# Optimization experiments

Measured on AMD Instinct MI355X. Metric: run time of the kernel, lower is better.

Reference implementation:

```python
import jax, jax.numpy as jnp
import numpy as np

L = 12; D = 768; H = 12; HD = D // H
P = 16; IMG = 224; NPATCH = (IMG // P) ** 2
NCLS = 1000; B = 32
GAMMA = 0.01; MIN_TOKENS = 16; EPS = 1e-6
SCALE = HD ** -0.5


def _ln(x, w, b, eps=1e-6):
    mu = x.mean(-1, keepdims=True)
    var = ((x - mu) ** 2).mean(-1, keepdims=True)
    return (x - mu) * jax.lax.rsqrt(var + eps) * w + b


def setup_inputs() -> dict:
    key = jax.random.key(0)
    ks = jax.random.split(key, 16)
    s = 0.02
    rn = lambda k, shape: jax.random.normal(k, shape, jnp.float32) * s
    return {
        'x': jax.random.normal(ks[0], (B, 3, IMG, IMG), jnp.float32),
        'patch_w': rn(ks[1], (D, 3, P, P)),
        'patch_b': jnp.zeros((D,), jnp.float32),
        'cls_token': rn(ks[2], (1, 1, D)),
        'pos_embed': rn(ks[3], (1, NPATCH + 1, D)),
        'ln1_w': jnp.ones((L, D), jnp.float32), 'ln1_b': jnp.zeros((L, D), jnp.float32),
        'qkv_w': rn(ks[4], (L, D, 3 * D)), 'qkv_b': jnp.zeros((L, 3 * D), jnp.float32),
        'proj_w': rn(ks[5], (L, D, D)), 'proj_b': jnp.zeros((L, D), jnp.float32),
        'ln2_w': jnp.ones((L, D), jnp.float32), 'ln2_b': jnp.zeros((L, D), jnp.float32),
        'fc1_w': rn(ks[6], (L, D, 4 * D)), 'fc1_b': jnp.zeros((L, 4 * D), jnp.float32),
        'fc2_w': rn(ks[7], (L, 4 * D, D)), 'fc2_b': jnp.zeros((L, D), jnp.float32),
        'norm_w': jnp.ones((D,), jnp.float32), 'norm_b': jnp.zeros((D,), jnp.float32),
        'head_w': rn(ks[8], (D, NCLS)), 'head_b': jnp.zeros((NCLS,), jnp.float32),
    }


def _block(x, i, ln1_w, ln1_b, qkv_w, qkv_b, proj_w, proj_b, ln2_w, ln2_b, fc1_w, fc1_b, fc2_w, fc2_b):
    Bb, Ntok, _ = x.shape
    xn = _ln(x, ln1_w[i], ln1_b[i])
    qkv = (xn @ qkv_w[i] + qkv_b[i]).reshape(Bb, Ntok, 3, H, HD)
    qkv = qkv.transpose(2, 0, 3, 1, 4)  # [3, B, H, N, hd]
    q, k, v = qkv[0], qkv[1], qkv[2]
    # full N x N attention matrix, materialized as in the original module
    attn = jax.nn.softmax(jnp.einsum('bhqd,bhkd->bhqk', q, k) * SCALE, axis=-1)
    out = jnp.einsum('bhqk,bhkd->bhqd', attn, v)
    out = out.transpose(0, 2, 1, 3).reshape(Bb, Ntok, D) @ proj_w[i] + proj_b[i]
    x = x + out
    h = _ln(x, ln2_w[i], ln2_b[i])
    h = jax.nn.gelu(h @ fc1_w[i] + fc1_b[i], approximate=False)
    x = x + (h @ fc2_w[i] + fc2_b[i])
    return x, attn, v


def _importance(attn, v, eps):
    # Jacobian proxy: d(CLS)/d(patch_j) ~ attn[CLS->j] * ||v_j||
    v_norm = jnp.linalg.norm(v, axis=-1)            # [B, H, N]
    jac = attn[:, :, 0, 1:] * v_norm[:, :, 1:]       # [B, H, Npatch]
    importance = jac.mean(axis=(0, 1))               # batch-shared [Npatch]
    mass = importance.sum()
    rho = importance.std() / (importance.mean() + eps)
    return importance, mass, rho


def _keep_ratio(rho, mass, prev_mass, gamma, eps):
    drift = jnp.abs(mass - prev_mass) / (prev_mass + eps)
    return jnp.clip(1.0 - gamma * rho * (1.0 + drift), 0.0, 1.0)


def _select(importance, n_keep):
    _, idx = jax.lax.top_k(importance, n_keep)
    idx = jnp.sort(idx) + 1  # shift past CLS
    return jnp.concatenate([jnp.zeros((1,), idx.dtype), idx])  # always keep CLS


def reference(x, patch_w, patch_b, cls_token, pos_embed, ln1_w, ln1_b, qkv_w, qkv_b,
              proj_w, proj_b, ln2_w, ln2_b, fc1_w, fc1_b, fc2_w, fc2_b,
              norm_w, norm_b, head_w, head_b):
    Bb = x.shape[0]
    feat = jax.lax.conv_general_dilated(x, patch_w, (P, P), 'VALID',
                                        dimension_numbers=('NCHW', 'OIHW', 'NCHW'))
    feat = feat.reshape(Bb, D, NPATCH).transpose(0, 2, 1) + patch_b  # [B, 196, D]
    xx = jnp.concatenate([jnp.broadcast_to(cls_token, (Bb, 1, D)), feat], axis=1) + pos_embed
    N = NPATCH
    prev_mass = None
    for i in range(L):
        xx, attn, v = _block(xx, i, ln1_w, ln1_b, qkv_w, qkv_b, proj_w, proj_b,
                             ln2_w, ln2_b, fc1_w, fc1_b, fc2_w, fc2_b)
        if N <= MIN_TOKENS:
            prev_mass = None
            continue
        imp, mass, rho = _importance(attn, v, EPS)
        if prev_mass is not None:
            kr = float(_keep_ratio(rho, mass, prev_mass, GAMMA, EPS))
            n_next = max(MIN_TOKENS, int(N * kr))
        else:
            n_next = N
        if n_next < N:
            keep_idx = _select(imp, n_next)
            xx = jnp.take(xx, keep_idx, axis=1)
            N = n_next
        prev_mass = mass
    xx = _ln(xx, norm_w, norm_b)
    return xx[:, 0] @ head_w + head_b
```

## Files before the change

kernel.cpp:

```cpp
#include <hip/hip_runtime.h>
#include <math.h>

#define DEV_INLINE __device__ __forceinline__

constexpr int BB     = 32;
constexpr int DMODEL = 768;
constexpr int NHEAD  = 12;
constexpr int NPATCH = 196;
constexpr int NTOK   = 197;
constexpr int NLAYER = 12;
constexpr int NCLASS = 1000;
constexpr int MTOT   = BB * NTOK;

typedef __attribute__((ext_vector_type(4))) float f32x4;
typedef __attribute__((ext_vector_type(8))) short bf16x8;

DEV_INLINE void split2(float x, unsigned short& hi, unsigned short& lo) {
    unsigned u = __builtin_bit_cast(unsigned, x);
    unsigned r = (u + 0x7FFFu + ((u >> 16) & 1u)) >> 16;
    hi = (unsigned short)r;
    float fh = __builtin_bit_cast(float, r << 16);
    float l = x - fh;
    unsigned ul = __builtin_bit_cast(unsigned, l);
    lo = (unsigned short)((ul + 0x7FFFu + ((ul >> 16) & 1u)) >> 16);
}

DEV_INLINE unsigned split_pack(float x) {
    unsigned short h, l; split2(x, h, l);
    return (unsigned)h | ((unsigned)l << 16);
}

DEV_INLINE void gload16(const unsigned short* g, unsigned short* l) {
    __builtin_amdgcn_global_load_lds(
        (const __attribute__((address_space(1))) unsigned int*)g,
        (__attribute__((address_space(3))) unsigned int*)l, 16, 0, 0);
}

DEV_INLINE float block_reduce_sum(float v, float* sbuf) {
    #pragma unroll
    for (int off = 32; off > 0; off >>= 1) v += __shfl_down(v, off, 64);
    int lane = threadIdx.x & 63, w = threadIdx.x >> 6;
    __syncthreads();
    if (lane == 0) sbuf[w] = v;
    __syncthreads();
    return sbuf[0] + sbuf[1] + sbuf[2] + sbuf[3];
}

__global__ void state_init(int* nTokPtr, int* prevValidPtr) {
    *nTokPtr = NTOK;
    *prevValidPtr = 0;
}

__global__ __launch_bounds__(256)
void cls_init(const float* __restrict__ cls, const float* __restrict__ pos,
              float* __restrict__ tok) {
    int b = blockIdx.x;
    for (int i = threadIdx.x; i < DMODEL; i += 256)
        tok[(size_t)b * NTOK * DMODEL + i] = cls[i] + pos[i];
}

__global__ __launch_bounds__(256)
void wconv_patch(const float* __restrict__ src, unsigned short* __restrict__ hi,
                 unsigned short* __restrict__ lo) {
    int id = blockIdx.x * 256 + threadIdx.x;
    if (id >= 768 * 96) return;
    int n = id / 96, ch = id % 96;
    int k = ch * 8;
    float4 a = *(const float4*)(src + (size_t)n * 768 + k);
    float4 b = *(const float4*)(src + (size_t)n * 768 + k + 4);
    unsigned short h[8], l[8];
    split2(a.x,h[0],l[0]); split2(a.y,h[1],l[1]); split2(a.z,h[2],l[2]); split2(a.w,h[3],l[3]);
    split2(b.x,h[4],l[4]); split2(b.y,h[5],l[5]); split2(b.z,h[6],l[6]); split2(b.w,h[7],l[7]);
    int npanel = n >> 7, c = n & 127;
    int kbi = k >> 5, chunk = (k >> 3) & 3;
    size_t base = ((size_t)npanel * 24 + kbi) * 4096
                + c * 32 + ((chunk ^ ((c >> 1) & 3)) << 3);
    bf16x8 hv, lv;
    #pragma unroll
    for (int j = 0; j < 8; ++j) { hv[j] = (short)h[j]; lv[j] = (short)l[j]; }
    *(bf16x8*)(hi + base) = hv;
    *(bf16x8*)(lo + base) = lv;
}

constexpr size_t WOFF_QKV  = 0;
constexpr size_t WOFF_PROJ = (size_t)768 * 2304;
constexpr size_t WOFF_FC1  = WOFF_PROJ + (size_t)768 * 768;
constexpr size_t WOFF_FC2  = WOFF_FC1 + (size_t)768 * 3072;
constexpr size_t WTOTAL    = WOFF_FC2 + (size_t)3072 * 768;

__global__ __launch_bounds__(256)
void wconv_layer(const float* __restrict__ qkvw, const float* __restrict__ projw,
                 const float* __restrict__ fc1w, const float* __restrict__ fc2w,
                 unsigned short* __restrict__ hi, unsigned short* __restrict__ lo) {
    __shared__ float tile[32][33];
    int bid = blockIdx.x;
    const float* src; int Kd, Nd; size_t dofs;
    if (bid < 1728)      { src = qkvw;  Kd = 768;  Nd = 2304; dofs = WOFF_QKV; }
    else if (bid < 2304) { bid -= 1728; src = projw; Kd = 768;  Nd = 768;  dofs = WOFF_PROJ; }
    else if (bid < 4608) { bid -= 2304; src = fc1w;  Kd = 768;  Nd = 3072; dofs = WOFF_FC1; }
    else                 { bid -= 4608; src = fc2w;  Kd = 3072; Nd = 768;  dofs = WOFF_FC2; }
    const int nkb = Kd >> 5;
    int ntx = Nd / 32;
    int n0 = (bid % ntx) * 32, k0 = (bid / ntx) * 32;
    int tx = threadIdx.x & 31, ty = threadIdx.x >> 5;
    #pragma unroll
    for (int i = 0; i < 32; i += 8)
        tile[ty + i][tx] = src[(size_t)(k0 + ty + i) * Nd + n0 + tx];
    __syncthreads();
    int t = threadIdx.x;
    if (t < 128) {
        int nl = t >> 2, chunk = t & 3;
        unsigned short h[8], l[8];
        #pragma unroll
        for (int j = 0; j < 8; ++j) split2(tile[chunk * 8 + j][nl], h[j], l[j]);
        int n = n0 + nl, k = k0 + chunk * 8;
        int npanel = n >> 7, c = n & 127;
        int kbi = k >> 5;
        size_t base = dofs + ((size_t)npanel * nkb + kbi) * 4096
                    + c * 32 + ((chunk ^ ((c >> 1) & 3)) << 3);
        bf16x8 hv, lv;
        #pragma unroll
        for (int j = 0; j < 8; ++j) { hv[j] = (short)h[j]; lv[j] = (short)l[j]; }
        *(bf16x8*)(hi + base) = hv;
        *(bf16x8*)(lo + base) = lv;
    }
}

template<int ASRC, int EPI>
__global__ __launch_bounds__(256)
void mfma_gemm(const void* __restrict__ A, int lda,
               const unsigned short* __restrict__ Wht,
               const unsigned short* __restrict__ Wlt,
               const float* __restrict__ bias,
               const float* __restrict__ resid,
               void* __restrict__ C, int ldc,
               int K, int Mtot, int gm, int gn,
               const int* __restrict__ nTokPtr) {
    const int nTok = (ASRC == 0) ? *nTokPtr : NTOK;
    int nb = gm * gn;
    int o = blockIdx.x;
    int q8 = nb >> 3, r8 = nb & 7;
    int xcd = o & 7, wi = o >> 3;
    int fin = (xcd < r8 ? xcd * (q8 + 1) : r8 * (q8 + 1) + (xcd - r8) * q8) + wi;
    int bm = fin / gn, bn = fin - bm * gn;
    const int m0 = bm * 128, n0 = bn * 128;
    if (m0 >= Mtot) return;
    if (ASRC == 0) {
        int ts = m0 % NTOK;
        if (!(ts < nTok || ts + 128 > NTOK)) return;
    }
    __shared__ unsigned short Ah[4096], Al[4096], Bh[4096], Bl[4096];
    const int tid = threadIdx.x;
    const int lane = tid & 63, wid = tid >> 6;
    const int wm = wid >> 1, wn = wid & 1;
    const int fr = lane & 15, fg = lane >> 4;

    f32x4 acc[4][4];
    #pragma unroll
    for (int i = 0; i < 4; ++i)
        #pragma unroll
        for (int j = 0; j < 4; ++j) acc[i][j] = (f32x4){0.f, 0.f, 0.f, 0.f};

    const int arow = tid >> 1;
    const int acp  = (tid & 1) * 2;
    const int am = m0 + arow;
    bool aval = am < Mtot;
    if (ASRC == 0) aval = aval && (am % NTOK) < nTok;
    size_t abase;
    if (ASRC == 0) abase = (size_t)am * lda;
    else {
        int b = am / NPATCH, pp = am - b * NPATCH;
        int py = pp / 14, px = pp - py * 14;
        abase = (size_t)b * (3 * 224 * 224) + (size_t)(py * 16) * 224 + px * 16;
    }
    const int axor = (arow >> 1) & 3;
    const int aoff0 = arow * 32 + ((acp ^ axor) << 3);
    const int aoff1 = arow * 32 + (((acp + 1) ^ axor) << 3);
    const int nkb = K >> 5;
    const int wbase = wid * 512;
    const int g8 = tid * 8;

    for (int kbi = 0; kbi < nkb; ++kbi) {
        const int kb = kbi << 5;
        {
            size_t tb = ((size_t)bn * nkb + kbi) * 4096;
            gload16(Wht + tb + g8,        &Bh[wbase]);
            gload16(Wht + tb + g8 + 2048, &Bh[wbase + 2048]);
            gload16(Wlt + tb + g8,        &Bl[wbase]);
            gload16(Wlt + tb + g8 + 2048, &Bl[wbase + 2048]);
        }
        unsigned ph[8], pl[8];
        if (ASRC == 0) {
            unsigned u[16] = {0,0,0,0,0,0,0,0,0,0,0,0,0,0,0,0};
            if (aval) {
                const unsigned* ap = (const unsigned*)A + abase + kb + acp * 8;
                *(uint4*)&u[0]  = *(const uint4*)ap;
                *(uint4*)&u[4]  = *(const uint4*)(ap + 4);
                *(uint4*)&u[8]  = *(const uint4*)(ap + 8);
                *(uint4*)&u[12] = *(const uint4*)(ap + 12);
            }
            #pragma unroll
            for (int j = 0; j < 8; ++j) {
                unsigned a = u[2 * j], b = u[2 * j + 1];
                ph[j] = (a & 0xffffu) | (b << 16);
                pl[j] = (a >> 16) | (b & 0xffff0000u);
            }
        } else {
            float f[16] = {0,0,0,0,0,0,0,0,0,0,0,0,0,0,0,0};
            if (aval) {
                int k = kb + acp * 8;
                size_t off = abase + (size_t)(k >> 8) * (224 * 224)
                           + (size_t)((k >> 4) & 15) * 224;
                *(float4*)&f[0]  = *(const float4*)((const float*)A + off);
                *(float4*)&f[4]  = *(const float4*)((const float*)A + off + 4);
                *(float4*)&f[8]  = *(const float4*)((const float*)A + off + 8);
                *(float4*)&f[12] = *(const float4*)((const float*)A + off + 12);
            }
            #pragma unroll
            for (int j = 0; j < 8; ++j) {
                unsigned short h0, l0, h1, l1;
                split2(f[2 * j], h0, l0); split2(f[2 * j + 1], h1, l1);
                ph[j] = (unsigned)h0 | ((unsigned)h1 << 16);
                pl[j] = (unsigned)l0 | ((unsigned)l1 << 16);
            }
        }
        *(uint4*)&Ah[aoff0] = *(uint4*)&ph[0];
        *(uint4*)&Ah[aoff1] = *(uint4*)&ph[4];
        *(uint4*)&Al[aoff0] = *(uint4*)&pl[0];
        *(uint4*)&Al[aoff1] = *(uint4*)&pl[4];
        __syncthreads();
        bf16x8 ah[4], al4[4], bh4[4], bl4[4];
        #pragma unroll
        for (int i = 0; i < 4; ++i) {
            int row = wm * 64 + i * 16 + fr;
            int aoff = row * 32 + ((fg ^ ((row >> 1) & 3)) << 3);
            ah[i]  = *(const bf16x8*)&Ah[aoff];
            al4[i] = *(const bf16x8*)&Al[aoff];
            int col = wn * 64 + i * 16 + fr;
            int boff = col * 32 + ((fg ^ ((col >> 1) & 3)) << 3);
            bh4[i] = *(const bf16x8*)&Bh[boff];
            bl4[i] = *(const bf16x8*)&Bl[boff];
        }
        #pragma unroll
        for (int i = 0; i < 4; ++i)
            #pragma unroll
            for (int j = 0; j < 4; ++j) {
                acc[i][j] = __builtin_amdgcn_mfma_f32_16x16x32_bf16(ah[i],  bh4[j], acc[i][j], 0, 0, 0);
                acc[i][j] = __builtin_amdgcn_mfma_f32_16x16x32_bf16(ah[i],  bl4[j], acc[i][j], 0, 0, 0);
                acc[i][j] = __builtin_amdgcn_mfma_f32_16x16x32_bf16(al4[i], bh4[j], acc[i][j], 0, 0, 0);
            }
        __syncthreads();
    }
    #pragma unroll
    for (int i = 0; i < 4; ++i) {
        #pragma unroll
        for (int j = 0; j < 4; ++j) {
            #pragma unroll
            for (int e = 0; e < 4; ++e) {
                int m = m0 + wm * 64 + i * 16 + fg * 4 + e;
                int n = n0 + wn * 64 + j * 16 + fr;
                if (m >= Mtot) continue;
                if (ASRC == 0 && (m % NTOK) >= nTok) continue;
                float v = acc[i][j][e] + bias[n];
                if constexpr (EPI == 0) {
                    ((float*)C)[(size_t)m * ldc + n] = v;
                } else if constexpr (EPI == 1) {
                    ((float*)C)[(size_t)m * ldc + n] = v + resid[(size_t)m * ldc + n];
                } else if constexpr (EPI == 2) {
                    v = 0.5f * v * (1.0f + erff(v * 0.70710678118654752f));
                    ((unsigned*)C)[(size_t)m * ldc + n] = split_pack(v);
                } else {
                    int b = m / NPATCH, pp = m - b * NPATCH;
                    v += resid[(size_t)(1 + pp) * DMODEL + n];
                    ((float*)C)[((size_t)b * NTOK + 1 + pp) * DMODEL + n] = v;
                }
            }
        }
    }
}

__global__ __launch_bounds__(256)
void ln_tok(const float* __restrict__ X, unsigned* __restrict__ Y,
            const float* __restrict__ w, const float* __restrict__ b,
            const int* __restrict__ nTokPtr) {
    int m = blockIdx.x;
    if ((m % NTOK) >= *nTokPtr) return;
    __shared__ float sbuf[4];
    const float* x = X + (size_t)m * DMODEL;
    int tid = threadIdx.x;
    float v[3];
    #pragma unroll
    for (int i = 0; i < 3; i++) v[i] = x[tid + i * 256];
    float mu = block_reduce_sum(v[0] + v[1] + v[2], sbuf) * (1.0f / 768.0f);
    float d2 = 0.f;
    #pragma unroll
    for (int i = 0; i < 3; i++) { float d = v[i] - mu; d2 = fmaf(d, d, d2); }
    float var = block_reduce_sum(d2, sbuf) * (1.0f / 768.0f);
    float rstd = rsqrtf(var + 1e-6f);
    #pragma unroll
    for (int i = 0; i < 3; i++) {
        int idx = tid + i * 256;
        float y = (v[i] - mu) * rstd * w[idx] + b[idx];
        Y[(size_t)m * DMODEL + idx] = split_pack(y);
    }
}

__global__ __launch_bounds__(256)
void ln_cls(const float* __restrict__ X, float* __restrict__ Y,
            const float* __restrict__ w, const float* __restrict__ b) {
    int bb = blockIdx.x;
    __shared__ float sbuf[4];
    const float* x = X + (size_t)bb * NTOK * DMODEL;
    int tid = threadIdx.x;
    float v[3];
    #pragma unroll
    for (int i = 0; i < 3; i++) v[i] = x[tid + i * 256];
    float mu = block_reduce_sum(v[0] + v[1] + v[2], sbuf) * (1.0f / 768.0f);
    float d2 = 0.f;
    #pragma unroll
    for (int i = 0; i < 3; i++) { float d = v[i] - mu; d2 = fmaf(d, d, d2); }
    float var = block_reduce_sum(d2, sbuf) * (1.0f / 768.0f);
    float rstd = rsqrtf(var + 1e-6f);
    #pragma unroll
    for (int i = 0; i < 3; i++) {
        int idx = tid + i * 256;
        Y[(size_t)bb * DMODEL + idx] = (v[i] - mu) * rstd * w[idx] + b[idx];
    }
}

__global__ __launch_bounds__(256)
void attn_v2(const float* __restrict__ qkv, unsigned* __restrict__ outu,
             float* __restrict__ jacg, const int* __restrict__ nTokPtr) {
    const int nTok = *nTokPtr;
    const int bh = blockIdx.x;
    const int b = bh / NHEAD, h = bh % NHEAD;
    const int q0 = blockIdx.y * 32;
    if (q0 >= nTok) return;
    __shared__ float Qs[32][68];
    __shared__ float KVs[64][68];
    __shared__ float Ss[32][67];
    __shared__ float mrow[32], lrow[32], frow[32];
    __shared__ float s0row[208];
    __shared__ float vnrow[208];
    const int tid = threadIdx.x;
    const float* base = qkv + (size_t)b * NTOK * 2304 + (size_t)h * 64;

    {
        int r = tid >> 3, fc = tid & 7;
        int q = q0 + r;
        #pragma unroll
        for (int p = 0; p < 2; ++p) {
            float4 v = make_float4(0.f, 0.f, 0.f, 0.f);
            if (q < nTok) v = *(const float4*)(base + (size_t)q * 2304 + (fc + p * 8) * 4);
            *(float4*)&Qs[r][(fc + p * 8) * 4] = v;
        }
    }
    if (tid < 32) { mrow[tid] = -INFINITY; lrow[tid] = 0.f; }

    float o[2][4] = {{0.f,0.f,0.f,0.f},{0.f,0.f,0.f,0.f}};
    const int qq = tid & 15, dd = tid >> 4;
    const int q2 = qq * 2;
    const int njt = (nTok + 63) >> 6;

    for (int jt = 0; jt < njt; ++jt) {
        const int jb = jt * 64;
        __syncthreads();
        {
            int jr = tid >> 2, fc = tid & 3;
            int j = jb + jr;
            const float* krow = base + (size_t)j * 2304 + 768;
            #pragma unroll
            for (int p = 0; p < 4; ++p) {
                float4 v = make_float4(0.f, 0.f, 0.f, 0.f);
                if (j < nTok) v = *(const float4*)(krow + (fc + p * 4) * 4);
                *(float4*)&KVs[jr][(fc + p * 4) * 4] = v;
            }
        }
        __syncthreads();
        {
            const int jj = tid >> 4;
            float sacc[2][4] = {{0,0,0,0},{0,0,0,0}};
            #pragma unroll 4
            for (int d0 = 0; d0 < 16; ++d0) {
                float4 qa = *(const float4*)&Qs[q2][d0 * 4];
                float4 qb = *(const float4*)&Qs[q2 + 1][d0 * 4];
                #pragma unroll
                for (int r = 0; r < 4; ++r) {
                    float4 kv = *(const float4*)&KVs[jj * 4 + r][d0 * 4];
                    sacc[0][r] = fmaf(qa.x, kv.x, sacc[0][r]);
                    sacc[0][r] = fmaf(qa.y, kv.y, sacc[0][r]);
                    sacc[0][r] = fmaf(qa.z, kv.z, sacc[0][r]);
                    sacc[0][r] = fmaf(qa.w, kv.w, sacc[0][r]);
                    sacc[1][r] = fmaf(qb.x, kv.x, sacc[1][r]);
                    sacc[1][r] = fmaf(qb.y, kv.y, sacc[1][r]);
                    sacc[1][r] = fmaf(qb.z, kv.z, sacc[1][r]);
                    sacc[1][r] = fmaf(qb.w, kv.w, sacc[1][r]);
                }
            }
            #pragma unroll
            for (int s = 0; s < 2; ++s) {
                int q = q0 + q2 + s;
                #pragma unroll
                for (int r = 0; r < 4; ++r) {
                    int j = jb + jj * 4 + r;
                    float sv = (j < nTok && q < nTok) ? sacc[s][r] * 0.125f : -INFINITY;
                    Ss[q2 + s][jj * 4 + r] = sv;
                    if (q0 == 0 && qq == 0 && s == 0 && j < nTok) s0row[j] = sv;
                }
            }
        }
        __syncthreads();
        if (tid < 32) {
            int q = q0 + tid;
            if (q < nTok) {
                int jn = min(64, nTok - jb);
                float mt = -INFINITY;
                for (int j = 0; j < jn; ++j) mt = fmaxf(mt, Ss[tid][j]);
                float mnew = fmaxf(mrow[tid], mt);
                float f = expf(mrow[tid] - mnew);
                float sum = 0.f;
                for (int j = 0; j < jn; ++j) {
                    float p = expf(Ss[tid][j] - mnew);
                    Ss[tid][j] = p; sum += p;
                }
                for (int j = jn; j < 64; ++j) Ss[tid][j] = 0.f;
                lrow[tid] = lrow[tid] * f + sum;
                mrow[tid] = mnew;
                frow[tid] = f;
            }
        }
        {
            int jr = tid >> 2, fc = tid & 3;
            int j = jb + jr;
            const float* vrow = base + (size_t)j * 2304 + 1536;
            #pragma unroll
            for (int p = 0; p < 4; ++p) {
                float4 v = make_float4(0.f, 0.f, 0.f, 0.f);
                if (j < nTok) v = *(const float4*)(vrow + (fc + p * 4) * 4);
                *(float4*)&KVs[jr][(fc + p * 4) * 4] = v;
            }
        }
        __syncthreads();
        if (q0 == 0 && tid < 64) {
            int j = jb + tid;
            if (j < nTok) {
                float s = 0.f;
                for (int d = 0; d < 64; ++d) { float v = KVs[tid][d]; s = fmaf(v, v, s); }
                vnrow[j] = sqrtf(s);
            }
        }
        {
            float f0 = frow[q2], f1 = frow[q2 + 1];
            #pragma unroll
            for (int r = 0; r < 4; ++r) { o[0][r] *= f0; o[1][r] *= f1; }
            for (int j = 0; j < 64; ++j) {
                float p0 = Ss[q2][j], p1 = Ss[q2 + 1][j];
                float4 vv = *(const float4*)&KVs[j][dd * 4];
                o[0][0] = fmaf(p0, vv.x, o[0][0]);
                o[0][1] = fmaf(p0, vv.y, o[0][1]);
                o[0][2] = fmaf(p0, vv.z, o[0][2]);
                o[0][3] = fmaf(p0, vv.w, o[0][3]);
                o[1][0] = fmaf(p1, vv.x, o[1][0]);
                o[1][1] = fmaf(p1, vv.y, o[1][1]);
                o[1][2] = fmaf(p1, vv.z, o[1][2]);
                o[1][3] = fmaf(p1, vv.w, o[1][3]);
            }
        }
    }
    __syncthreads();
    #pragma unroll
    for (int s = 0; s < 2; ++s) {
        int q = q0 + q2 + s;
        if (q < nTok) {
            float inv = 1.0f / lrow[q2 + s];
            uint4 pv;
            pv.x = split_pack(o[s][0] * inv);
            pv.y = split_pack(o[s][1] * inv);
            pv.z = split_pack(o[s][2] * inv);
            pv.w = split_pack(o[s][3] * inv);
            *(uint4*)(outu + ((size_t)b * NTOK + q) * DMODEL + (size_t)h * 64 + dd * 4) = pv;
        }
    }
    if (q0 == 0) {
        float m0f = mrow[0], l0 = lrow[0];
        for (int j = 1 + tid; j < nTok; j += 256)
            jacg[(size_t)bh * NPATCH + (j - 1)] = (expf(s0row[j] - m0f) / l0) * vnrow[j];
    }
}

__global__ __launch_bounds__(256)
void decide_kernel(const float* __restrict__ jac,
                   int* __restrict__ nTokPtr, int* __restrict__ nTokNextPtr,
                   int* __restrict__ keepIdx, float* __restrict__ prevMassPtr,
                   int* __restrict__ prevValidPtr) {
    const int nTok = *nTokPtr;
    const int N = nTok - 1;
    const int tid = threadIdx.x;
    if (N <= 16) {
        if (tid == 0) { *prevValidPtr = 0; *nTokNextPtr = nTok; }
        for (int t = tid; t < nTok; t += 256) keepIdx[t] = t;
        return;
    }
    __shared__ float impF[NPATCH];
    __shared__ int   sel[NPATCH];
    __shared__ int   s_next;
    for (int j = tid; j < N; j += 256) {
        double s = 0.0;
        for (int r = 0; r < BB * NHEAD; r++) s += (double)jac[(size_t)r * NPATCH + j];
        impF[j] = (float)(s * (1.0 / 384.0));
    }
    __syncthreads();
    if (tid == 0) {
        double ms = 0.0;
        for (int j = 0; j < N; j++) ms += (double)impF[j];
        float massF = (float)ms;
        float meanF = (float)(ms / (double)N);
        double vs = 0.0;
        for (int j = 0; j < N; j++) { double d = (double)impF[j] - (double)meanF; vs += d * d; }
        float stdF = (float)sqrt(vs / (double)N);
        float rho = stdF / (meanF + 1e-6f);
        int nnext;
        if (*prevValidPtr != 0) {
            float pm = *prevMassPtr;
            float drift = fabsf(massF - pm) / (pm + 1e-6f);
            float kr = 1.0f - 0.01f * rho * (1.0f + drift);
            kr = fminf(fmaxf(kr, 0.0f), 1.0f);
            int t = (int)((double)N * (double)kr);
            nnext = t < 16 ? 16 : t;
        } else {
            nnext = N;
        }
        *prevMassPtr = massF;
        *prevValidPtr = 1;
        s_next = nnext;
        *nTokNextPtr = nnext + 1;
    }
    __syncthreads();
    int nnext = s_next;
    if (nnext < N) {
        for (int j = tid; j < N; j += 256) {
            float vj = impF[j];
            int rank = 0;
            for (int i = 0; i < N; i++) {
                float vi = impF[i];
                rank += (vi > vj || (vi == vj && i < j)) ? 1 : 0;
            }
            sel[j] = (rank < nnext) ? 1 : 0;
        }
        __syncthreads();
        if (tid == 0) {
            int c = 1;
            keepIdx[0] = 0;
            for (int j = 0; j < N; j++) if (sel[j]) keepIdx[c++] = j + 1;
        }
    } else {
        for (int t = tid; t < nTok; t += 256) keepIdx[t] = t;
    }
}

__global__ __launch_bounds__(192)
void gather_kernel(const float* __restrict__ src, float* __restrict__ dst,
                   const int* __restrict__ keepIdx,
                   const int* __restrict__ nTokNextPtr, int* __restrict__ nTokPtr) {
    int nn = *nTokNextPtr;
    int m = blockIdx.x;
    int b = m / NTOK, t = m - b * NTOK;
    if (t < nn) {
        int s = keepIdx[t];
        const float4* sp = (const float4*)(src + ((size_t)b * NTOK + s) * DMODEL);
        float4* dp = (float4*)(dst + ((size_t)b * NTOK + t) * DMODEL);
        dp[threadIdx.x] = sp[threadIdx.x];
    }
    if (m == 0 && threadIdx.x == 0) *nTokPtr = nn;
}

__global__ __launch_bounds__(256)
void head_kernel(const float* __restrict__ lnC, const float* __restrict__ W,
                 const float* __restrict__ hb, float* __restrict__ out) {
    int b = blockIdx.x;
    int n = blockIdx.y * 256 + threadIdx.x;
    __shared__ float xs[DMODEL];
    for (int i = threadIdx.x; i < DMODEL; i += 256) xs[i] = lnC[(size_t)b * DMODEL + i];
    __syncthreads();
    if (n < NCLASS) {
        float acc = hb[n];
        for (int d = 0; d < DMODEL; d++) acc = fmaf(xs[d], W[(size_t)d * NCLASS + n], acc);
        out[(size_t)b * NCLASS + n] = acc;
    }
}

extern "C" void kernel_launch(void* const* d_in, const int* in_sizes, int n_in,
                              void* d_out, int out_size, void* d_ws, size_t ws_size,
                              hipStream_t stream) {
    const float* x       = (const float*)d_in[0];
    const float* patch_w = (const float*)d_in[1];
    const float* patch_b = (const float*)d_in[2];
    const float* cls_tok = (const float*)d_in[3];
    const float* pos     = (const float*)d_in[4];
    const float* ln1_w   = (const float*)d_in[5];
    const float* ln1_b   = (const float*)d_in[6];
    const float* qkv_w   = (const float*)d_in[7];
    const float* qkv_b   = (const float*)d_in[8];
    const float* proj_w  = (const float*)d_in[9];
    const float* proj_b  = (const float*)d_in[10];
    const float* ln2_w   = (const float*)d_in[11];
    const float* ln2_b   = (const float*)d_in[12];
    const float* fc1_w   = (const float*)d_in[13];
    const float* fc1_b   = (const float*)d_in[14];
    const float* fc2_w   = (const float*)d_in[15];
    const float* fc2_b   = (const float*)d_in[16];
    const float* norm_w  = (const float*)d_in[17];
    const float* norm_b  = (const float*)d_in[18];
    const float* head_w  = (const float*)d_in[19];
    const float* head_b  = (const float*)d_in[20];
    float* out = (float*)d_out;

    char* ws = (char*)d_ws;
    size_t off = 0;
    auto alloc = [&](size_t nbytes) {
        char* p = ws + off;
        off += ((nbytes + 255) / 256) * 256;
        return p;
    };
    float* tokA = (float*)alloc((size_t)MTOT * DMODEL * 4);
    float* tokB = (float*)alloc((size_t)MTOT * DMODEL * 4);
    char* uni = alloc((size_t)MTOT * 3072 * 4);
    float* qkvb = (float*)uni;
    unsigned* hbu = (unsigned*)uni;
    unsigned* xnu  = (unsigned*)alloc((size_t)MTOT * DMODEL * 4);
    unsigned* outu = (unsigned*)alloc((size_t)MTOT * DMODEL * 4);
    unsigned short* whi = (unsigned short*)alloc(WTOTAL * 2);
    unsigned short* wlo = (unsigned short*)alloc(WTOTAL * 2);
    unsigned short* wphi = (unsigned short*)alloc((size_t)768 * 768 * 2);
    unsigned short* wplo = (unsigned short*)alloc((size_t)768 * 768 * 2);
    float* jac  = (float*)alloc((size_t)BB * NHEAD * NPATCH * 4);
    float* lnC  = (float*)alloc((size_t)BB * DMODEL * 4);
    float* prevMass = (float*)alloc(32);
    int* ints = (int*)alloc(1024);
    int* nTokP = ints; int* nTokNextP = ints + 1; int* prevValidP = ints + 2;
    int* keepIdx = ints + 4;

    dim3 blk(256);
    state_init<<<dim3(1), dim3(1), 0, stream>>>(nTokP, prevValidP);
    wconv_patch<<<dim3(288), blk, 0, stream>>>(patch_w, wphi, wplo);
    cls_init<<<dim3(BB), blk, 0, stream>>>(cls_tok, pos, tokA);
    mfma_gemm<1, 3><<<dim3(49 * 6), blk, 0, stream>>>(
        x, 0, wphi, wplo, patch_b, pos, tokA, DMODEL, 768, BB * NPATCH, 49, 6, nTokP);

    float* bufs[2] = {tokA, tokB};
    const int gm = (MTOT + 127) / 128;
    for (int l = 0; l < NLAYER; l++) {
        float* cur = bufs[l & 1];
        float* nxt = bufs[(l + 1) & 1];
        wconv_layer<<<dim3(6912), blk, 0, stream>>>(
            qkv_w + (size_t)l * 768 * 2304, proj_w + (size_t)l * 768 * 768,
            fc1_w + (size_t)l * 768 * 3072, fc2_w + (size_t)l * 3072 * 768, whi, wlo);
        ln_tok<<<dim3(MTOT), blk, 0, stream>>>(cur, xnu, ln1_w + l * 768, ln1_b + l * 768, nTokP);
        mfma_gemm<0, 0><<<dim3(gm * 18), blk, 0, stream>>>(
            xnu, 768, whi + WOFF_QKV, wlo + WOFF_QKV, qkv_b + (size_t)l * 2304,
            nullptr, qkvb, 2304, 768, MTOT, gm, 18, nTokP);
        attn_v2<<<dim3(BB * NHEAD, 7), blk, 0, stream>>>(qkvb, outu, jac, nTokP);
        mfma_gemm<0, 1><<<dim3(gm * 6), blk, 0, stream>>>(
            outu, 768, whi + WOFF_PROJ, wlo + WOFF_PROJ, proj_b + (size_t)l * 768,
            cur, cur, 768, 768, MTOT, gm, 6, nTokP);
        ln_tok<<<dim3(MTOT), blk, 0, stream>>>(cur, xnu, ln2_w + l * 768, ln2_b + l * 768, nTokP);
        mfma_gemm<0, 2><<<dim3(gm * 24), blk, 0, stream>>>(
            xnu, 768, whi + WOFF_FC1, wlo + WOFF_FC1, fc1_b + (size_t)l * 3072,
            nullptr, hbu, 3072, 768, MTOT, gm, 24, nTokP);
        mfma_gemm<0, 1><<<dim3(gm * 6), blk, 0, stream>>>(
            hbu, 3072, whi + WOFF_FC2, wlo + WOFF_FC2, fc2_b + (size_t)l * 768,
            cur, cur, 768, 3072, MTOT, gm, 6, nTokP);
        decide_kernel<<<dim3(1), blk, 0, stream>>>(jac, nTokP, nTokNextP, keepIdx,
                                                   prevMass, prevValidP);
        gather_kernel<<<dim3(MTOT), dim3(192), 0, stream>>>(cur, nxt, keepIdx, nTokNextP, nTokP);
    }
    ln_cls<<<dim3(BB), blk, 0, stream>>>(bufs[0], lnC, norm_w, norm_b);
    head_kernel<<<dim3(BB, 4), blk, 0, stream>>>(lnC, head_w, head_b, out);
}
```

Measured before the change: 7.432 ms.

## Move attention QK and PV products onto bf16x3 MFMA with packed split inputs

The QKV GEMM epilogue now writes each value as a packed bf16 hi/lo pair, and the attention kernel is rewritten to compute QK^T and PV with 16x16x32 bf16 MFMA using a three-product split for near-fp32 accuracy. K and V are staged together in swizzled shared memory, with V transposed. Softmax is spread across all threads with shuffle reductions, and the V-norm computation is folded into the load phase. This is meant to replace scalar FMA attention loops with matrix-core work and cut barrier-heavy serial softmax, at the cost of more shared memory and the precision limits of the split-bf16 scheme.

Result: faster. 6.455 ms (-13.1%).

```diff
diff --git a/kernel.cpp b/kernel.cpp
--- a/kernel.cpp
+++ b/kernel.cpp
@@ -263,7 +263,7 @@
                 if (ASRC == 0 && (m % NTOK) >= nTok) continue;
                 float v = acc[i][j][e] + bias[n];
                 if constexpr (EPI == 0) {
-                    ((float*)C)[(size_t)m * ldc + n] = v;
+                    ((unsigned*)C)[(size_t)m * ldc + n] = split_pack(v);
                 } else if constexpr (EPI == 1) {
                     ((float*)C)[(size_t)m * ldc + n] = v + resid[(size_t)m * ldc + n];
                 } else if constexpr (EPI == 2) {
@@ -329,156 +329,221 @@
 }
 
 __global__ __launch_bounds__(256)
-void attn_v2(const float* __restrict__ qkv, unsigned* __restrict__ outu,
+void attn_v3(const unsigned* __restrict__ qkv, unsigned* __restrict__ outu,
              float* __restrict__ jacg, const int* __restrict__ nTokPtr) {
     const int nTok = *nTokPtr;
     const int bh = blockIdx.x;
     const int b = bh / NHEAD, h = bh % NHEAD;
     const int q0 = blockIdx.y * 32;
     if (q0 >= nTok) return;
-    __shared__ float Qs[32][68];
-    __shared__ float KVs[64][68];
-    __shared__ float Ss[32][67];
+    __shared__ unsigned short Kh[64 * 64], Kl[64 * 64];
+    __shared__ unsigned short Vth[64 * 64], Vtl[64 * 64];
+    __shared__ unsigned short Ph[32 * 64], Pl[32 * 64];
+    __shared__ float Ss[32][68];
     __shared__ float mrow[32], lrow[32], frow[32];
-    __shared__ float s0row[208];
-    __shared__ float vnrow[208];
+    __shared__ float s0row[256], vnrow[256];
+    __shared__ float vnpart[64][4];
     const int tid = threadIdx.x;
-    const float* base = qkv + (size_t)b * NTOK * 2304 + (size_t)h * 64;
+    const int lane = tid & 63, wv = tid >> 6;
+    const int fr = lane & 15, fg = lane >> 4;
+    const int qh = wv >> 1, xh = wv & 1;
+    const unsigned* base = qkv + (size_t)b * NTOK * 2304 + (size_t)h * 64;
 
     {
+        unsigned* Qu = (unsigned*)&Ss[0][0];
         int r = tid >> 3, fc = tid & 7;
         int q = q0 + r;
+        uint4 v = make_uint4(0,0,0,0), w = make_uint4(0,0,0,0);
+        if (q < nTok) {
+            v = *(const uint4*)(base + (size_t)q * 2304 + fc * 8);
+            w = *(const uint4*)(base + (size_t)q * 2304 + fc * 8 + 4);
+        }
+        *(uint4*)&Qu[r * 68 + fc * 8] = v;
+        *(uint4*)&Qu[r * 68 + fc * 8 + 4] = w;
+    }
+    if (tid < 32) { mrow[tid] = -INFINITY; lrow[tid] = 0.f; frow[tid] = 1.f; }
+    __syncthreads();
+    bf16x8 qah[2], qal[2];
+    {
+        const unsigned* Qu = (const unsigned*)&Ss[0][0];
+        int r = qh * 16 + fr;
         #pragma unroll
-        for (int p = 0; p < 2; ++p) {
-            float4 v = make_float4(0.f, 0.f, 0.f, 0.f);
-            if (q < nTok) v = *(const float4*)(base + (size_t)q * 2304 + (fc + p * 8) * 4);
-            *(float4*)&Qs[r][(fc + p * 8) * 4] = v;
-        }
-    }
-    if (tid < 32) { mrow[tid] = -INFINITY; lrow[tid] = 0.f; }
-
-    float o[2][4] = {{0.f,0.f,0.f,0.f},{0.f,0.f,0.f,0.f}};
-    const int qq = tid & 15, dd = tid >> 4;
-    const int q2 = qq * 2;
+        for (int s = 0; s < 2; ++s)
+            #pragma unroll
+            for (int i = 0; i < 8; ++i) {
+                unsigned u = Qu[r * 68 + s * 32 + fg * 8 + i];
+                qah[s][i] = (short)(u & 0xffffu);
+                qal[s][i] = (short)(u >> 16);
+            }
+    }
+    f32x4 oacc[2] = {{0,0,0,0},{0,0,0,0}};
     const int njt = (nTok + 63) >> 6;
+    const int sj = tid & 63, sdh = tid >> 6;
 
     for (int jt = 0; jt < njt; ++jt) {
         const int jb = jt * 64;
         __syncthreads();
         {
-            int jr = tid >> 2, fc = tid & 3;
-            int j = jb + jr;
-            const float* krow = base + (size_t)j * 2304 + 768;
-            #pragma unroll
-            for (int p = 0; p < 4; ++p) {
-                float4 v = make_float4(0.f, 0.f, 0.f, 0.f);
-                if (j < nTok) v = *(const float4*)(krow + (fc + p * 4) * 4);
-                *(float4*)&KVs[jr][(fc + p * 4) * 4] = v;
-            }
+            int j = jb + sj;
+            uint4 ku[4], vu[4];
+            if (j < nTok) {
+                const unsigned* kr = base + (size_t)j * 2304 + 768 + sdh * 16;
+                const unsigned* vr = base + (size_t)j * 2304 + 1536 + sdh * 16;
+                ku[0] = *(const uint4*)kr;       ku[1] = *(const uint4*)(kr + 4);
+                ku[2] = *(const uint4*)(kr + 8); ku[3] = *(const uint4*)(kr + 12);
+                vu[0] = *(const uint4*)vr;       vu[1] = *(const uint4*)(vr + 4);
+                vu[2] = *(const uint4*)(vr + 8); vu[3] = *(const uint4*)(vr + 12);
+            } else {
+                ku[0]=ku[1]=ku[2]=ku[3] = make_uint4(0,0,0,0);
+                vu[0]=vu[1]=vu[2]=vu[3] = make_uint4(0,0,0,0);
+            }
+            const unsigned* kw = (const unsigned*)ku;
+            bf16x8 kh0, kh1, kl0, kl1;
+            #pragma unroll
+            for (int i = 0; i < 8; ++i) {
+                kh0[i] = (short)(kw[i] & 0xffffu);     kl0[i] = (short)(kw[i] >> 16);
+                kh1[i] = (short)(kw[8 + i] & 0xffffu); kl1[i] = (short)(kw[8 + i] >> 16);
+            }
+            int c0 = sdh * 2;
+            int ko0 = sj * 64 + ((c0 ^ (sj & 7)) << 3);
+            int ko1 = sj * 64 + (((c0 + 1) ^ (sj & 7)) << 3);
+            *(bf16x8*)&Kh[ko0] = kh0; *(bf16x8*)&Kh[ko1] = kh1;
+            *(bf16x8*)&Kl[ko0] = kl0; *(bf16x8*)&Kl[ko1] = kl1;
+            const unsigned* vw = (const unsigned*)vu;
+            float pn = 0.f;
+            #pragma unroll
+            for (int i = 0; i < 16; ++i) {
+                unsigned u = vw[i];
+                int d = sdh * 16 + i;
+                int si = d * 64 + (((sj >> 3) ^ (d & 7)) << 3) + (sj & 7);
+                Vth[si] = (unsigned short)(u & 0xffffu);
+                Vtl[si] = (unsigned short)(u >> 16);
+                if (q0 == 0) {
+                    float vf = __builtin_bit_cast(float, u << 16)
+                             + __builtin_bit_cast(float, u & 0xffff0000u);
+                    pn = fmaf(vf, vf, pn);
+                }
+            }
+            if (q0 == 0) vnpart[sj][sdh] = pn;
         }
         __syncthreads();
         {
-            const int jj = tid >> 4;
-            float sacc[2][4] = {{0,0,0,0},{0,0,0,0}};
-            #pragma unroll 4
-            for (int d0 = 0; d0 < 16; ++d0) {
-                float4 qa = *(const float4*)&Qs[q2][d0 * 4];
-                float4 qb = *(const float4*)&Qs[q2 + 1][d0 * 4];
+            f32x4 sacc[2] = {{0,0,0,0},{0,0,0,0}};
+            #pragma unroll
+            for (int s = 0; s < 2; ++s)
                 #pragma unroll
-                for (int r = 0; r < 4; ++r) {
-                    float4 kv = *(const float4*)&KVs[jj * 4 + r][d0 * 4];
-                    sacc[0][r] = fmaf(qa.x, kv.x, sacc[0][r]);
-                    sacc[0][r] = fmaf(qa.y, kv.y, sacc[0][r]);
-                    sacc[0][r] = fmaf(qa.z, kv.z, sacc[0][r]);
-                    sacc[0][r] = fmaf(qa.w, kv.w, sacc[0][r]);
-                    sacc[1][r] = fmaf(qb.x, kv.x, sacc[1][r]);
-                    sacc[1][r] = fmaf(qb.y, kv.y, sacc[1][r]);
-                    sacc[1][r] = fmaf(qb.z, kv.z, sacc[1][r]);
-                    sacc[1][r] = fmaf(qb.w, kv.w, sacc[1][r]);
+                for (int t = 0; t < 2; ++t) {
+                    int j = xh * 32 + t * 16 + fr;
+                    int off = j * 64 + (((s * 4 + fg) ^ (j & 7)) << 3);
+                    bf16x8 kbh = *(const bf16x8*)&Kh[off];
+                    bf16x8 kbl = *(const bf16x8*)&Kl[off];
+                    sacc[t] = __builtin_amdgcn_mfma_f32_16x16x32_bf16(qah[s], kbh, sacc[t], 0, 0, 0);
+                    sacc[t] = __builtin_amdgcn_mfma_f32_16x16x32_bf16(qah[s], kbl, sacc[t], 0, 0, 0);
+                    sacc[t] = __builtin_amdgcn_mfma_f32_16x16x32_bf16(qal[s], kbh, sacc[t], 0, 0, 0);
                 }
-            }
+            #pragma unroll
+            for (int t = 0; t < 2; ++t)
+                #pragma unroll
+                for (int e = 0; e < 4; ++e) {
+                    int q = q0 + qh * 16 + fg * 4 + e;
+                    int j = jb + xh * 32 + t * 16 + fr;
+                    Ss[qh * 16 + fg * 4 + e][xh * 32 + t * 16 + fr] =
+                        (q < nTok && j < nTok) ? sacc[t][e] * 0.125f : -INFINITY;
+                }
+        }
+        __syncthreads();
+        {
+            int q = tid >> 3, s = tid & 7;
+            bool rowok = (q0 + q) < nTok;
+            float4 va = *(const float4*)&Ss[q][s * 8];
+            float4 vb = *(const float4*)&Ss[q][s * 8 + 4];
+            if (q0 == 0 && q == 0) {
+                *(float4*)&s0row[jb + s * 8] = va;
+                *(float4*)&s0row[jb + s * 8 + 4] = vb;
+            }
+            float mx = fmaxf(fmaxf(fmaxf(va.x, va.y), fmaxf(va.z, va.w)),
+                             fmaxf(fmaxf(vb.x, vb.y), fmaxf(vb.z, vb.w)));
+            #pragma unroll
+            for (int o = 1; o < 8; o <<= 1) mx = fmaxf(mx, __shfl_xor(mx, o));
+            float mold = mrow[q];
+            float mnew = fmaxf(mold, mx);
+            float e[8];
+            float sum = 0.f;
+            if (rowok) {
+                e[0] = expf(va.x - mnew); e[1] = expf(va.y - mnew);
+                e[2] = expf(va.z - mnew); e[3] = expf(va.w - mnew);
+                e[4] = expf(vb.x - mnew); e[5] = expf(vb.y - mnew);
+                e[6] = expf(vb.z - mnew); e[7] = expf(vb.w - mnew);
+                sum = ((e[0] + e[1]) + (e[2] + e[3])) + ((e[4] + e[5]) + (e[6] + e[7]));
+            } else {
+                #pragma unroll
+                for (int i = 0; i < 8; ++i) e[i] = 0.f;
+            }
+            #pragma unroll
+            for (int o = 1; o < 8; o <<= 1) sum += __shfl_xor(sum, o);
+            bf16x8 ph, pl;
+            #pragma unroll
+            for (int i = 0; i < 8; ++i) {
+                unsigned u = __builtin_bit_cast(unsigned, e[i]);
+                ph[i] = (short)(u >> 16);
+                float r = e[i] - __builtin_bit_cast(float, u & 0xffff0000u);
+                pl[i] = (short)(__builtin_bit_cast(unsigned, r) >> 16);
+            }
+            int poff = q * 64 + ((s ^ (q & 7)) << 3);
+            *(bf16x8*)&Ph[poff] = ph;
+            *(bf16x8*)&Pl[poff] = pl;
+            if (s == 0 && rowok) {
+                float f = expf(mold - mnew);
+                lrow[q] = lrow[q] * f + sum;
+                mrow[q] = mnew;
+                frow[q] = f;
+            }
+            if (q0 == 0 && tid < 64) {
+                int jj = jb + tid;
+                if (jj < nTok)
+                    vnrow[jj] = sqrtf(vnpart[tid][0] + vnpart[tid][1]
+                                    + vnpart[tid][2] + vnpart[tid][3]);
+            }
+        }
+        __syncthreads();
+        {
+            float fe[4];
+            #pragma unroll
+            for (int e = 0; e < 4; ++e) fe[e] = frow[qh * 16 + fg * 4 + e];
+            #pragma unroll
+            for (int t = 0; t < 2; ++t)
+                #pragma unroll
+                for (int e = 0; e < 4; ++e) oacc[t][e] *= fe[e];
             #pragma unroll
             for (int s = 0; s < 2; ++s) {
-                int q = q0 + q2 + s;
+                int pr = qh * 16 + fr;
+                int poff = pr * 64 + (((s * 4 + fg) ^ (pr & 7)) << 3);
+                bf16x8 pah = *(const bf16x8*)&Ph[poff];
+                bf16x8 pal = *(const bf16x8*)&Pl[poff];
                 #pragma unroll
-                for (int r = 0; r < 4; ++r) {
-                    int j = jb + jj * 4 + r;
-                    float sv = (j < nTok && q < nTok) ? sacc[s][r] * 0.125f : -INFINITY;
-                    Ss[q2 + s][jj * 4 + r] = sv;
-                    if (q0 == 0 && qq == 0 && s == 0 && j < nTok) s0row[j] = sv;
+                for (int t = 0; t < 2; ++t) {
+                    int d = xh * 32 + t * 16 + fr;
+                    int voff = d * 64 + (((s * 4 + fg) ^ (d & 7)) << 3);
+                    bf16x8 vbh = *(const bf16x8*)&Vth[voff];
+                    bf16x8 vbl = *(const bf16x8*)&Vtl[voff];
+                    oacc[t] = __builtin_amdgcn_mfma_f32_16x16x32_bf16(pah, vbh, oacc[t], 0, 0, 0);
+                    oacc[t] = __builtin_amdgcn_mfma_f32_16x16x32_bf16(pah, vbl, oacc[t], 0, 0, 0);
+                    oacc[t] = __builtin_amdgcn_mfma_f32_16x16x32_bf16(pal, vbh, oacc[t], 0, 0, 0);
                 }
             }
         }
-        __syncthreads();
-        if (tid < 32) {
-            int q = q0 + tid;
-            if (q < nTok) {
-                int jn = min(64, nTok - jb);
-                float mt = -INFINITY;
-                for (int j = 0; j < jn; ++j) mt = fmaxf(mt, Ss[tid][j]);
-                float mnew = fmaxf(mrow[tid], mt);
-                float f = expf(mrow[tid] - mnew);
-                float sum = 0.f;
-                for (int j = 0; j < jn; ++j) {
-                    float p = expf(Ss[tid][j] - mnew);
-                    Ss[tid][j] = p; sum += p;
-                }
-                for (int j = jn; j < 64; ++j) Ss[tid][j] = 0.f;
-                lrow[tid] = lrow[tid] * f + sum;
-                mrow[tid] = mnew;
-                frow[tid] = f;
-            }
-        }
-        {
-            int jr = tid >> 2, fc = tid & 3;
-            int j = jb + jr;
-            const float* vrow = base + (size_t)j * 2304 + 1536;
-            #pragma unroll
-            for (int p = 0; p < 4; ++p) {
-                float4 v = make_float4(0.f, 0.f, 0.f, 0.f);
-                if (j < nTok) v = *(const float4*)(vrow + (fc + p * 4) * 4);
-                *(float4*)&KVs[jr][(fc + p * 4) * 4] = v;
-            }
-        }
-        __syncthreads();
-        if (q0 == 0 && tid < 64) {
-            int j = jb + tid;
-            if (j < nTok) {
-                float s = 0.f;
-                for (int d = 0; d < 64; ++d) { float v = KVs[tid][d]; s = fmaf(v, v, s); }
-                vnrow[j] = sqrtf(s);
-            }
-        }
-        {
-            float f0 = frow[q2], f1 = frow[q2 + 1];
-            #pragma unroll
-            for (int r = 0; r < 4; ++r) { o[0][r] *= f0; o[1][r] *= f1; }
-            for (int j = 0; j < 64; ++j) {
-                float p0 = Ss[q2][j], p1 = Ss[q2 + 1][j];
-                float4 vv = *(const float4*)&KVs[j][dd * 4];
-                o[0][0] = fmaf(p0, vv.x, o[0][0]);
-                o[0][1] = fmaf(p0, vv.y, o[0][1]);
-                o[0][2] = fmaf(p0, vv.z, o[0][2]);
-                o[0][3] = fmaf(p0, vv.w, o[0][3]);
-                o[1][0] = fmaf(p1, vv.x, o[1][0]);
-                o[1][1] = fmaf(p1, vv.y, o[1][1]);
-                o[1][2] = fmaf(p1, vv.z, o[1][2]);
-                o[1][3] = fmaf(p1, vv.w, o[1][3]);
-            }
-        }
-    }
-    __syncthreads();
-    #pragma unroll
-    for (int s = 0; s < 2; ++s) {
-        int q = q0 + q2 + s;
+    }
+    #pragma unroll
+    for (int e = 0; e < 4; ++e) {
+        int qr = qh * 16 + fg * 4 + e;
+        int q = q0 + qr;
         if (q < nTok) {
-            float inv = 1.0f / lrow[q2 + s];
-            uint4 pv;
-            pv.x = split_pack(o[s][0] * inv);
-            pv.y = split_pack(o[s][1] * inv);
-            pv.z = split_pack(o[s][2] * inv);
-            pv.w = split_pack(o[s][3] * inv);
-            *(uint4*)(outu + ((size_t)b * NTOK + q) * DMODEL + (size_t)h * 64 + dd * 4) = pv;
+            float inv = 1.0f / lrow[qr];
+            #pragma unroll
+            for (int t = 0; t < 2; ++t) {
+                int n = h * 64 + xh * 32 + t * 16 + fr;
+                outu[((size_t)b * NTOK + q) * DMODEL + n] = split_pack(oacc[t][e] * inv);
+            }
         }
     }
     if (q0 == 0) {
@@ -625,7 +690,7 @@
     float* tokA = (float*)alloc((size_t)MTOT * DMODEL * 4);
     float* tokB = (float*)alloc((size_t)MTOT * DMODEL * 4);
     char* uni = alloc((size_t)MTOT * 3072 * 4);
-    float* qkvb = (float*)uni;
+    unsigned* qkvb = (unsigned*)uni;
     unsigned* hbu = (unsigned*)uni;
     unsigned* xnu  = (unsigned*)alloc((size_t)MTOT * DMODEL * 4);
     unsigned* outu = (unsigned*)alloc((size_t)MTOT * DMODEL * 4);
@@ -659,7 +724,7 @@
         mfma_gemm<0, 0><<<dim3(gm * 18), blk, 0, stream>>>(
             xnu, 768, whi + WOFF_QKV, wlo + WOFF_QKV, qkv_b + (size_t)l * 2304,
             nullptr, qkvb, 2304, 768, MTOT, gm, 18, nTokP);
-        attn_v2<<<dim3(BB * NHEAD, 7), blk, 0, stream>>>(qkvb, outu, jac, nTokP);
+        attn_v3<<<dim3(BB * NHEAD, 7), blk, 0, stream>>>(qkvb, outu, jac, nTokP);
         mfma_gemm<0, 1><<<dim3(gm * 6), blk, 0, stream>>>(
             outu, 768, whi + WOFF_PROJ, wlo + WOFF_PROJ, proj_b + (size_t)l * 768,
             cur, cur, 768, 768, MTOT, gm, 6, nTokP);
```
